# Optimization experiments

Hardware: AMD Instinct MI355X
Metric: run time of the kernel (lower is better)

The kernel has to match this reference:

```python
import jax, jax.numpy as jnp
import numpy as np

N_NODES = 50000
N_EDGES = 800000
X_DIM = 32
S_DIM = 16
H_DIM = 96   # = 2 * (X_DIM + S_DIM), edge-MLP input
O_DIM = 64


def setup_inputs() -> dict:
    key = jax.random.key(0)
    ks = jax.random.split(key, 6)
    x = jax.random.normal(ks[0], (N_NODES, X_DIM), dtype=jnp.float32)
    scalars = jax.random.normal(ks[1], (1, S_DIM), dtype=jnp.float32)
    W1 = jax.random.normal(ks[2], (H_DIM, H_DIM), dtype=jnp.float32) * (1.0 / np.sqrt(H_DIM))
    b1 = jnp.zeros((H_DIM,), dtype=jnp.float32)
    W2 = jax.random.normal(ks[3], (H_DIM, O_DIM), dtype=jnp.float32) * (1.0 / np.sqrt(H_DIM))
    b2 = jnp.zeros((O_DIM,), dtype=jnp.float32)
    edge_index = jax.random.randint(ks[4], (2, N_EDGES), 0, N_NODES, dtype=jnp.int64)
    return {"x": x, "scalars": scalars, "W1": W1, "b1": b1, "W2": W2,
            "b2": b2, "edge_index": edge_index}


def reference(x, scalars, W1, b1, W2, b2, edge_index):
    n = x.shape[0]
    # single-graph branch of EFN: expand scalars to every node, concat
    s = jnp.broadcast_to(scalars.reshape(1, -1), (n, scalars.shape[-1]))
    h = jnp.concatenate([x, s], axis=1)                      # [N, 48]
    src, dst = edge_index[0], edge_index[1]
    # PTConv: edge-wise MLP on cat([x_i, x_j - x_i]), sum-aggregate to i (dst)
    h_i = h[dst]                                             # [E, 48] gather
    h_j = h[src]                                             # [E, 48] gather
    m_in = jnp.concatenate([h_i, h_j - h_i], axis=1)         # [E, 96]
    m = jax.nn.relu(m_in @ W1 + b1) @ W2 + b2                # [E, 64]
    out = jax.ops.segment_sum(m, dst, num_segments=n)        # [N, 64] scatter-add
    return out
```

## Files before the change

kernel.cpp:

```cpp
#include <hip/hip_runtime.h>


typedef _Float16 half8 __attribute__((ext_vector_type(8)));
typedef _Float16 half2t __attribute__((ext_vector_type(2)));
typedef float f32x4 __attribute__((ext_vector_type(4)));
typedef float f32x2 __attribute__((ext_vector_type(2)));

#define LDK 72
#define LDW2 104
#define LDH 104
#define BCAP 1024
#define NBMAX 1563

static __device__ __forceinline__ unsigned char f32_to_fp8(float v) {
    int p = __builtin_amdgcn_cvt_pk_fp8_f32(v, v, 0, false);
    return (unsigned char)(p & 0xff);
}

__global__ __launch_bounds__(256) void prep_kernel(
    const float* __restrict__ x, const float* __restrict__ scalars,
    const float* __restrict__ W1, const float* __restrict__ b1,
    _Float16* __restrict__ Pbuf, unsigned char* __restrict__ Qf8,
    const int* __restrict__ src, const int* __restrict__ dst,
    int* __restrict__ bcur, unsigned int* __restrict__ pairs,
    int tiles, int n_e4, int epb4, int nb, int nplace)
{
    __shared__ union {
        struct { int h[NBMAX]; int cur[NBMAX]; } pl;
        _Float16 sW[192 * LDK];
    } sm;
    const int tid = threadIdx.x;

    if ((int)blockIdx.x < nplace) {
        int* h = sm.pl.h;
        int* cur = sm.pl.cur;
        for (int b = tid; b < nb; b += 256) h[b] = 0;
        __syncthreads();

        const int base4 = blockIdx.x * epb4;
        for (int i = tid; i < epb4; i += 256) {
            int i4 = base4 + i;
            if (i4 < n_e4) {
                int4 d = ((const int4*)dst)[i4];
                atomicAdd(&h[d.x >> 5], 1);
                atomicAdd(&h[d.y >> 5], 1);
                atomicAdd(&h[d.z >> 5], 1);
                atomicAdd(&h[d.w >> 5], 1);
            }
        }
        __syncthreads();
        for (int b = tid; b < nb; b += 256) {
            int c = h[b];
            cur[b] = b * BCAP + (c ? atomicAdd(&bcur[b], c) : 0);
        }
        __syncthreads();
        for (int i = tid; i < epb4; i += 256) {
            int i4 = base4 + i;
            if (i4 < n_e4) {
                int4 s = ((const int4*)src)[i4];
                int4 d = ((const int4*)dst)[i4];
                int p;
                p = atomicAdd(&cur[d.x >> 5], 1);
                if (p < (d.x >> 5) * BCAP + BCAP) pairs[p] = (unsigned)s.x | ((unsigned)(d.x & 31) << 16);
                p = atomicAdd(&cur[d.y >> 5], 1);
                if (p < (d.y >> 5) * BCAP + BCAP) pairs[p] = (unsigned)s.y | ((unsigned)(d.y & 31) << 16);
                p = atomicAdd(&cur[d.z >> 5], 1);
                if (p < (d.z >> 5) * BCAP + BCAP) pairs[p] = (unsigned)s.z | ((unsigned)(d.z & 31) << 16);
                p = atomicAdd(&cur[d.w >> 5], 1);
                if (p < (d.w >> 5) * BCAP + BCAP) pairs[p] = (unsigned)s.w | ((unsigned)(d.w & 31) << 16);
            }
        }
    } else {
        _Float16* sW = sm.sW;
        for (int idx = tid; idx < 192 * 64; idx += 256) {
            int n = idx >> 6, k = idx & 63;
            float v = 0.f;
            if (k < 48)
                v = (n < 96) ? (W1[k * 96 + n] - W1[(k + 48) * 96 + n])
                             : W1[(k + 48) * 96 + (n - 96)];
            sW[n * LDK + k] = (_Float16)v;
        }
        __syncthreads();

        const int wave = tid >> 6, lane = tid & 63;
        const int quad = lane >> 4, r = lane & 15;
        const int pb = blockIdx.x - nplace;
        const int stride = (gridDim.x - nplace) * 4;

        for (int tile = pb * 4 + wave; tile < tiles; tile += stride) {
            const int node = tile * 16 + r;

            half8 a0, a1;
            {
                const float* xp = x + (size_t)node * 32 + quad * 8;
                #pragma unroll
                for (int j = 0; j < 8; ++j) a0[j] = (_Float16)xp[j];
                #pragma unroll
                for (int j = 0; j < 8; ++j) {
                    int k2 = 32 + quad * 8 + j;
                    a1[j] = (k2 < 48) ? (_Float16)scalars[k2 - 32] : (_Float16)0.f;
                }
            }

            #pragma unroll
            for (int nt = 0; nt < 12; ++nt) {
                f32x4 c = {0.f, 0.f, 0.f, 0.f};
                half8 b0 = *(const half8*)&sW[(nt * 16 + r) * LDK + quad * 8];
                half8 b1v = *(const half8*)&sW[(nt * 16 + r) * LDK + 32 + quad * 8];
                c = __builtin_amdgcn_mfma_f32_16x16x32_f16(a0, b0, c, 0, 0, 0);
                c = __builtin_amdgcn_mfma_f32_16x16x32_f16(a1, b1v, c, 0, 0, 0);
                if (nt < 6) {
                    int col = nt * 16 + r;
                    float bb = b1[col];
                    #pragma unroll
                    for (int i = 0; i < 4; ++i)
                        Pbuf[(size_t)(tile * 16 + quad * 4 + i) * 96 + col] = (_Float16)(c[i] + bb);
                } else {
                    int col = (nt - 6) * 16 + r;
                    #pragma unroll
                    for (int i = 0; i < 4; ++i)
                        Qf8[(size_t)(tile * 16 + quad * 4 + i) * 96 + col] = f32_to_fp8(c[i]);
                }
            }
        }
    }
}

static __device__ __forceinline__ void acc_edge(
    float* __restrict__ ac, const float* __restrict__ pf,
    unsigned int q0, unsigned int q1, unsigned int q2)
{
    f32x2 v;
    v = __builtin_amdgcn_cvt_pk_f32_fp8((int)q0, false);
    { float t0 = pf[0] + v[0], t1 = pf[1] + v[1];
      ac[0] += t0 > 0.f ? t0 : 0.f; ac[1] += t1 > 0.f ? t1 : 0.f; }
    v = __builtin_amdgcn_cvt_pk_f32_fp8((int)q0, true);
    { float t0 = pf[2] + v[0], t1 = pf[3] + v[1];
      ac[2] += t0 > 0.f ? t0 : 0.f; ac[3] += t1 > 0.f ? t1 : 0.f; }
    v = __builtin_amdgcn_cvt_pk_f32_fp8((int)q1, false);
    { float t0 = pf[4] + v[0], t1 = pf[5] + v[1];
      ac[4] += t0 > 0.f ? t0 : 0.f; ac[5] += t1 > 0.f ? t1 : 0.f; }
    v = __builtin_amdgcn_cvt_pk_f32_fp8((int)q1, true);
    { float t0 = pf[6] + v[0], t1 = pf[7] + v[1];
      ac[6] += t0 > 0.f ? t0 : 0.f; ac[7] += t1 > 0.f ? t1 : 0.f; }
    v = __builtin_amdgcn_cvt_pk_f32_fp8((int)q2, false);
    { float t0 = pf[8] + v[0], t1 = pf[9] + v[1];
      ac[8] += t0 > 0.f ? t0 : 0.f; ac[9] += t1 > 0.f ? t1 : 0.f; }
    v = __builtin_amdgcn_cvt_pk_f32_fp8((int)q2, true);
    { float t0 = pf[10] + v[0], t1 = pf[11] + v[1];
      ac[10] += t0 > 0.f ? t0 : 0.f; ac[11] += t1 > 0.f ? t1 : 0.f; }
}

__global__ __launch_bounds__(256) void sgo_kernel(
    const _Float16* __restrict__ Pbuf, const unsigned char* __restrict__ Qf8,
    const int* __restrict__ bcur, const unsigned int* __restrict__ pairs,
    const float* __restrict__ W2, const float* __restrict__ b2,
    float* __restrict__ out, int n_nodes)
{
    __shared__ unsigned short s_sorted[BCAP];
    __shared__ _Float16 sW2T[64 * LDW2];
    __shared__ _Float16 sH[32 * LDH];
    __shared__ int s_cnt[32];
    __shared__ int s_off[33];
    __shared__ int s_cur[32];

    const int b = blockIdx.x;
    const int tid = threadIdx.x;
    const int lo_g = b * BCAP;
    int cnt = bcur[b];
    if (cnt > BCAP) cnt = BCAP;

    for (int idx = tid; idx < 96 * 64; idx += 256) {
        int k = idx / 64, n = idx - k * 64;
        sW2T[n * LDW2 + k] = (_Float16)W2[idx];
    }
    if (tid < 32) s_cnt[tid] = 0;
    __syncthreads();

    for (int i = tid; i < cnt; i += 256)
        atomicAdd(&s_cnt[(pairs[lo_g + i] >> 16) & 31], 1);
    __syncthreads();
    if (tid == 0) {
        int a = 0;
        #pragma unroll
        for (int l = 0; l < 32; ++l) { s_off[l] = a; a += s_cnt[l]; }
        s_off[32] = a;
    }
    __syncthreads();
    if (tid < 32) s_cur[tid] = s_off[tid];
    __syncthreads();
    for (int i = tid; i < cnt; i += 256) {
        unsigned int u = pairs[lo_g + i];
        int p = atomicAdd(&s_cur[(u >> 16) & 31], 1);
        s_sorted[p] = (unsigned short)(u & 0xffffu);
    }
    __syncthreads();

    const int wave = tid >> 6, lane = tid & 63;
    const int g = lane >> 3, j = lane & 7;
    const int ni = wave * 8 + g;
    const int node = b * 32 + ni;

    if (node < n_nodes) {
        const int lo = s_off[ni], hi = s_off[ni + 1];

        float pf[12];
        {
            const unsigned int* Pp = (const unsigned int*)(Pbuf + (size_t)node * 96);
            #pragma unroll
            for (int t = 0; t < 6; ++t) {
                half2t h = __builtin_bit_cast(half2t, Pp[j * 6 + t]);
                pf[2 * t] = (float)h[0];
                pf[2 * t + 1] = (float)h[1];
            }
        }

        float ac[12];
        #pragma unroll
        for (int k = 0; k < 12; ++k) ac[k] = 0.f;

        int i = lo;
        for (; i + 1 < hi; i += 2) {
            int s0 = s_sorted[i];
            int s1 = s_sorted[i + 1];
            const unsigned int* Q0 = (const unsigned int*)(Qf8 + (size_t)s0 * 96);
            const unsigned int* Q1 = (const unsigned int*)(Qf8 + (size_t)s1 * 96);
            unsigned int a0 = Q0[j * 3 + 0], a1 = Q0[j * 3 + 1], a2 = Q0[j * 3 + 2];
            unsigned int c0 = Q1[j * 3 + 0], c1 = Q1[j * 3 + 1], c2 = Q1[j * 3 + 2];
            acc_edge(ac, pf, a0, a1, a2);
            acc_edge(ac, pf, c0, c1, c2);
        }
        if (i < hi) {
            int s0 = s_sorted[i];
            const unsigned int* Q0 = (const unsigned int*)(Qf8 + (size_t)s0 * 96);
            acc_edge(ac, pf, Q0[j * 3 + 0], Q0[j * 3 + 1], Q0[j * 3 + 2]);
        }

        unsigned int* Hp = (unsigned int*)sH + ni * (LDH / 2);
        #pragma unroll
        for (int t = 0; t < 6; ++t) {
            half2t hv;
            hv[0] = (_Float16)ac[2 * t];
            hv[1] = (_Float16)ac[2 * t + 1];
            Hp[j * 6 + t] = __builtin_bit_cast(unsigned int, hv);
        }
    }
    __syncthreads();

    const int quad = lane >> 4, r = lane & 15;
    const int t = wave >> 1;
    const int nt0 = (wave & 1) * 2;

    half8 a[3];
    #pragma unroll
    for (int kk = 0; kk < 3; ++kk)
        a[kk] = *(const half8*)&sH[(t * 16 + r) * LDH + kk * 32 + quad * 8];

    #pragma unroll
    for (int w = 0; w < 2; ++w) {
        const int nt = nt0 + w;
        f32x4 c = {0.f, 0.f, 0.f, 0.f};
        #pragma unroll
        for (int kk = 0; kk < 3; ++kk) {
            half8 bfrag = *(const half8*)&sW2T[(nt * 16 + r) * LDW2 + kk * 32 + quad * 8];
            c = __builtin_amdgcn_mfma_f32_16x16x32_f16(a[kk], bfrag, c, 0, 0, 0);
        }
        const int col = nt * 16 + r;
        const float bb = b2[col];
        #pragma unroll
        for (int i = 0; i < 4; ++i) {
            int local = t * 16 + quad * 4 + i;
            int nd = b * 32 + local;
            if (nd < n_nodes) {
                int dg = s_off[local + 1] - s_off[local];
                out[(size_t)nd * 64 + col] = c[i] + dg * bb;
            }
        }
    }
}

extern "C" void kernel_launch(void* const* d_in, const int* in_sizes, int n_in,
                              void* d_out, int out_size, void* d_ws, size_t ws_size,
                              hipStream_t stream) {
    const float* x       = (const float*)d_in[0];
    const float* scalars = (const float*)d_in[1];
    const float* W1      = (const float*)d_in[2];
    const float* b1      = (const float*)d_in[3];
    const float* W2      = (const float*)d_in[4];
    const float* b2      = (const float*)d_in[5];
    const int*   ei      = (const int*)d_in[6];
    float* out = (float*)d_out;

    const int n_edges = in_sizes[6] / 2;
    const int n_nodes = in_sizes[0] / 32;
    const int* src = ei;
    const int* dst = ei + n_edges;
    const int nb = (n_nodes + 31) / 32;
    const int tiles = n_nodes / 16;

    char* w = (char*)d_ws;
    _Float16* Pbuf = (_Float16*)w;          w += (size_t)n_nodes * 96 * 2;
    unsigned char* Qf8 = (unsigned char*)w; w += (size_t)n_nodes * 96;
    unsigned int* pairs = (unsigned int*)w; w += (size_t)nb * BCAP * 4;
    int* bcur = (int*)w;                    w += (size_t)nb * 4;

    hipMemsetAsync(bcur, 0, (size_t)nb * 4, stream);

    const int nplace = 160;
    const int n_e4 = n_edges / 4;
    const int epb4 = (n_e4 + nplace - 1) / nplace;
    prep_kernel<<<dim3(256), dim3(256), 0, stream>>>(
        x, scalars, W1, b1, Pbuf, Qf8, src, dst, bcur, pairs,
        tiles, n_e4, epb4, nb, nplace);

    sgo_kernel<<<dim3(nb), dim3(256), 0, stream>>>(
        Pbuf, Qf8, bcur, pairs, W2, b2, out, n_nodes);
}
```

Before: 126.3 us.

## Split each node bucket across two blocks and two lane-groups per node

```diff
diff --git a/kernel.cpp b/kernel.cpp
--- a/kernel.cpp
+++ b/kernel.cpp
@@ -10,6 +10,7 @@
 #define LDW2 104
 #define LDH 104
 #define BCAP 1024
+#define HCAP 512
 #define NBMAX 1563
 
 static __device__ __forceinline__ unsigned char f32_to_fp8(float v) {
@@ -157,14 +158,16 @@
     const float* __restrict__ W2, const float* __restrict__ b2,
     float* __restrict__ out, int n_nodes)
 {
-    __shared__ unsigned short s_sorted[BCAP];
+    __shared__ unsigned short s_sorted[HCAP];
     __shared__ _Float16 sW2T[64 * LDW2];
-    __shared__ _Float16 sH[32 * LDH];
-    __shared__ int s_cnt[32];
-    __shared__ int s_off[33];
-    __shared__ int s_cur[32];
-
-    const int b = blockIdx.x;
+    __shared__ _Float16 sH[16 * LDH];
+    __shared__ int s_cnt[16];
+    __shared__ int s_off[17];
+    __shared__ int s_cur[16];
+
+    const int hb = blockIdx.x;
+    const int b = hb >> 1;
+    const int hsel = hb & 1;
     const int tid = threadIdx.x;
     const int lo_g = b * BCAP;
     int cnt = bcur[b];
@@ -174,32 +177,40 @@
         int k = idx / 64, n = idx - k * 64;
         sW2T[n * LDW2 + k] = (_Float16)W2[idx];
     }
-    if (tid < 32) s_cnt[tid] = 0;
-    __syncthreads();
-
-    for (int i = tid; i < cnt; i += 256)
-        atomicAdd(&s_cnt[(pairs[lo_g + i] >> 16) & 31], 1);
+    if (tid < 16) s_cnt[tid] = 0;
+    __syncthreads();
+
+    for (int i = tid; i < cnt; i += 256) {
+        unsigned int u = pairs[lo_g + i];
+        int l = (u >> 16) & 31;
+        if ((l >> 4) == hsel) atomicAdd(&s_cnt[l & 15], 1);
+    }
     __syncthreads();
     if (tid == 0) {
         int a = 0;
         #pragma unroll
-        for (int l = 0; l < 32; ++l) { s_off[l] = a; a += s_cnt[l]; }
-        s_off[32] = a;
-    }
-    __syncthreads();
-    if (tid < 32) s_cur[tid] = s_off[tid];
+        for (int l = 0; l < 16; ++l) { s_off[l] = a; a += s_cnt[l]; }
+        s_off[16] = a;
+    }
+    __syncthreads();
+    if (tid < 16) s_cur[tid] = s_off[tid];
     __syncthreads();
     for (int i = tid; i < cnt; i += 256) {
         unsigned int u = pairs[lo_g + i];
-        int p = atomicAdd(&s_cur[(u >> 16) & 31], 1);
-        s_sorted[p] = (unsigned short)(u & 0xffffu);
+        int l = (u >> 16) & 31;
+        if ((l >> 4) == hsel) {
+            int p = atomicAdd(&s_cur[l & 15], 1);
+            if (p < HCAP) s_sorted[p] = (unsigned short)(u & 0xffffu);
+        }
     }
     __syncthreads();
 
     const int wave = tid >> 6, lane = tid & 63;
     const int g = lane >> 3, j = lane & 7;
-    const int ni = wave * 8 + g;
-    const int node = b * 32 + ni;
+    const int gid = wave * 8 + g;
+    const int ni = gid >> 1;
+    const int par = gid & 1;
+    const int node = b * 32 + hsel * 16 + ni;
 
     if (node < n_nodes) {
         const int lo = s_off[ni], hi = s_off[ni + 1];
@@ -219,10 +230,10 @@
         #pragma unroll
         for (int k = 0; k < 12; ++k) ac[k] = 0.f;
 
-        int i = lo;
-        for (; i + 1 < hi; i += 2) {
+        int i = lo + par;
+        for (; i + 2 < hi; i += 4) {
             int s0 = s_sorted[i];
-            int s1 = s_sorted[i + 1];
+            int s1 = s_sorted[i + 2];
             const unsigned int* Q0 = (const unsigned int*)(Qf8 + (size_t)s0 * 96);
             const unsigned int* Q1 = (const unsigned int*)(Qf8 + (size_t)s1 * 96);
             unsigned int a0 = Q0[j * 3 + 0], a1 = Q0[j * 3 + 1], a2 = Q0[j * 3 + 2];
@@ -236,45 +247,45 @@
             acc_edge(ac, pf, Q0[j * 3 + 0], Q0[j * 3 + 1], Q0[j * 3 + 2]);
         }
 
-        unsigned int* Hp = (unsigned int*)sH + ni * (LDH / 2);
         #pragma unroll
-        for (int t = 0; t < 6; ++t) {
-            half2t hv;
-            hv[0] = (_Float16)ac[2 * t];
-            hv[1] = (_Float16)ac[2 * t + 1];
-            Hp[j * 6 + t] = __builtin_bit_cast(unsigned int, hv);
+        for (int k = 0; k < 12; ++k)
+            ac[k] += __shfl_xor(ac[k], 8);
+
+        if (par == 0) {
+            unsigned int* Hp = (unsigned int*)sH + ni * (LDH / 2);
+            #pragma unroll
+            for (int t = 0; t < 6; ++t) {
+                half2t hv;
+                hv[0] = (_Float16)ac[2 * t];
+                hv[1] = (_Float16)ac[2 * t + 1];
+                Hp[j * 6 + t] = __builtin_bit_cast(unsigned int, hv);
+            }
         }
     }
     __syncthreads();
 
     const int quad = lane >> 4, r = lane & 15;
-    const int t = wave >> 1;
-    const int nt0 = (wave & 1) * 2;
 
     half8 a[3];
     #pragma unroll
     for (int kk = 0; kk < 3; ++kk)
-        a[kk] = *(const half8*)&sH[(t * 16 + r) * LDH + kk * 32 + quad * 8];
-
+        a[kk] = *(const half8*)&sH[r * LDH + kk * 32 + quad * 8];
+
+    f32x4 c = {0.f, 0.f, 0.f, 0.f};
     #pragma unroll
-    for (int w = 0; w < 2; ++w) {
-        const int nt = nt0 + w;
-        f32x4 c = {0.f, 0.f, 0.f, 0.f};
-        #pragma unroll
-        for (int kk = 0; kk < 3; ++kk) {
-            half8 bfrag = *(const half8*)&sW2T[(nt * 16 + r) * LDW2 + kk * 32 + quad * 8];
-            c = __builtin_amdgcn_mfma_f32_16x16x32_f16(a[kk], bfrag, c, 0, 0, 0);
-        }
-        const int col = nt * 16 + r;
-        const float bb = b2[col];
-        #pragma unroll
-        for (int i = 0; i < 4; ++i) {
-            int local = t * 16 + quad * 4 + i;
-            int nd = b * 32 + local;
-            if (nd < n_nodes) {
-                int dg = s_off[local + 1] - s_off[local];
-                out[(size_t)nd * 64 + col] = c[i] + dg * bb;
-            }
+    for (int kk = 0; kk < 3; ++kk) {
+        half8 bfrag = *(const half8*)&sW2T[(wave * 16 + r) * LDW2 + kk * 32 + quad * 8];
+        c = __builtin_amdgcn_mfma_f32_16x16x32_f16(a[kk], bfrag, c, 0, 0, 0);
+    }
+    const int col = wave * 16 + r;
+    const float bb = b2[col];
+    #pragma unroll
+    for (int i = 0; i < 4; ++i) {
+        int local = quad * 4 + i;
+        int nd = b * 32 + hsel * 16 + local;
+        if (nd < n_nodes) {
+            int dg = s_off[local + 1] - s_off[local];
+            out[(size_t)nd * 64 + col] = c[i] + dg * bb;
         }
     }
 }
@@ -313,6 +324,6 @@
         x, scalars, W1, b1, Pbuf, Qf8, src, dst, bcur, pairs,
         tiles, n_e4, epb4, nb, nplace);
 
-    sgo_kernel<<<dim3(nb), dim3(256), 0, stream>>>(
+    sgo_kernel<<<dim3(nb * 2), dim3(256), 0, stream>>>(
         Pbuf, Qf8, bcur, pairs, W2, b2, out, n_nodes);
 }
```

After: 129.1 us. +2.2%, slower.
